# Optimization experiments

Measured on AMD Instinct MI355X. Metric: run time of the kernel, lower is better.

Reference implementation:

```python
import jax, jax.numpy as jnp
import numpy as np

S, B, D, H, E, K = 1024, 4, 1024, 16, 3, 2
DFF = 4 * D
DH = D // H


def _layernorm(x, w, b, eps=1e-5):
    mu = jnp.mean(x, axis=-1, keepdims=True)
    var = jnp.var(x, axis=-1, keepdims=True)
    return (x - mu) * jax.lax.rsqrt(var + eps) * w + b


def _quick_gelu(x):
    return x * jax.nn.sigmoid(1.702 * x)


def setup_inputs() -> dict:
    key = jax.random.key(0)
    ks = jax.random.split(key, 8)
    w = lambda k, shape: jax.random.normal(k, shape, dtype=jnp.float32) * 0.02
    return {
        "x": jax.random.normal(ks[0], (S, B, D), dtype=jnp.float32),
        "ln1_w": jnp.ones((D,), jnp.float32), "ln1_b": jnp.zeros((D,), jnp.float32),
        "ln2_w": jnp.ones((D,), jnp.float32), "ln2_b": jnp.zeros((D,), jnp.float32),
        "in_proj_w": w(ks[1], (3 * D, D)), "in_proj_b": jnp.zeros((3 * D,), jnp.float32),
        "out_proj_w": w(ks[2], (D, D)), "out_proj_b": jnp.zeros((D,), jnp.float32),
        "gate_w": w(ks[3], (E, D)),
        "fc_w": w(ks[4], (E, DFF, D)), "fc_b": jnp.zeros((E, DFF), jnp.float32),
        "proj_w": w(ks[5], (E, D, DFF)), "proj_b": jnp.zeros((E, D), jnp.float32),
    }


def _forward(x, ln1_w, ln1_b, ln2_w, ln2_b, in_proj_w, in_proj_b,
             out_proj_w, out_proj_b, gate_w, fc_w, fc_b, proj_w, proj_b):
    s, b, d = x.shape
    # --- causal self-attention (torch nn.MultiheadAttention, seq-first) ---
    h = _layernorm(x, ln1_w, ln1_b)
    qkv = h @ in_proj_w.T + in_proj_b                      # [S,B,3D]
    q, k, v = jnp.split(qkv, 3, axis=-1)
    to_bhsd = lambda t: t.reshape(s, b, H, DH).transpose(1, 2, 0, 3)  # [B,H,S,Dh]
    q, k, v = to_bhsd(q) * (DH ** -0.5), to_bhsd(k), to_bhsd(v)
    mask = jnp.where(jnp.arange(s)[:, None] >= jnp.arange(s)[None, :], 0.0, -jnp.inf)
    scores = jnp.einsum("bhqd,bhkd->bhqk", q, k) + mask    # [B,H,S,S]
    attn = jax.nn.softmax(scores, axis=-1)
    o = jnp.einsum("bhqk,bhkd->bhqd", attn, v)
    o = o.transpose(2, 0, 1, 3).reshape(s, b, d)
    x = x + (o @ out_proj_w.T + out_proj_b)

    # --- MoE routing ---
    hs = _layernorm(x, ln2_w, ln2_b)
    hs_flat = hs.reshape(-1, d)                            # [T,D], T = S*B
    router_logits = hs_flat @ gate_w.T                     # [T,E]
    rw = jax.nn.softmax(router_logits.astype(jnp.float32), axis=-1)
    top_vals, top_idx = jax.lax.top_k(rw, K)               # [T,K]
    top_vals = top_vals / jnp.sum(top_vals, axis=-1, keepdims=True)

    # dense grouped expert FFN (E=3 small, compute-all + masked combine)
    h1 = _quick_gelu(jnp.einsum("td,efd->etf", hs_flat, fc_w) + fc_b[:, None, :])
    expert_out = jnp.einsum("etf,edf->etd", h1, proj_w) + proj_b[:, None, :]  # [E,T,D]
    comb = jnp.sum(jax.nn.one_hot(top_idx, E, dtype=top_vals.dtype) * top_vals[..., None], axis=1)  # [T,E]
    final_hidden_states = jnp.einsum("te,etd->td", comb, expert_out).reshape(s, b, d)
    del final_hidden_states  # NOTE: source computes this but never uses it in the output

    gate_score = jnp.max(top_vals, axis=-1).reshape(s, b, 1)
    out = x * gate_score
    return out, router_logits


def reference(x, ln1_w, ln1_b, ln2_w, ln2_b, in_proj_w, in_proj_b,
              out_proj_w, out_proj_b, gate_w, fc_w, fc_b, proj_w, proj_b):
    return _forward(x, ln1_w, ln1_b, ln2_w, ln2_b, in_proj_w, in_proj_b,
                    out_proj_w, out_proj_b, gate_w, fc_w, fc_b, proj_w, proj_b)
```

## Files before the change

kernel.cpp:

```cpp
#include <hip/hip_runtime.h>
#include <hip/hip_bf16.h>

#define S_DIM 1024
#define B_DIM 4
#define D_DIM 1024
#define H_DIM 16
#define DH    64
#define T_DIM (S_DIM * B_DIM)
#define QKV_N (3 * D_DIM)

using bf16 = __hip_bfloat16;
typedef __attribute__((ext_vector_type(4))) float fx4;
typedef __attribute__((ext_vector_type(8))) short bx8;

__device__ __forceinline__ unsigned short f2bf(float f) {
  union { float f; unsigned int u; } cv; cv.f = f;
  unsigned int u = cv.u;
  unsigned int r = (u + 0x7FFFu + ((u >> 16) & 1u)) >> 16;
  return (unsigned short)r;
}

__device__ __forceinline__ void g2l16(const void* g, void* l) {
  __builtin_amdgcn_global_load_lds(
      (const __attribute__((address_space(1))) unsigned int*)g,
      (__attribute__((address_space(3))) unsigned int*)l, 16, 0, 0);
}

__global__ __launch_bounds__(256) void cast2_f32_bf16(
    const float* __restrict__ a, bf16* __restrict__ da, int an4,
    const float* __restrict__ b, bf16* __restrict__ db, int bn4) {
  const int i = blockIdx.x * 256 + threadIdx.x;
  const float* src; bf16* dst; int j;
  if (i < an4) { src = a; dst = da; j = i; }
  else if (i < an4 + bn4) { src = b; dst = db; j = i - an4; }
  else return;
  const fx4 v = ((const fx4*)src)[j];
  ushort4 u;
  u.x = f2bf(v[0]); u.y = f2bf(v[1]); u.z = f2bf(v[2]); u.w = f2bf(v[3]);
  ((ushort4*)dst)[j] = u;
}

__global__ __launch_bounds__(256) void ln_bf16_kernel(
    const float* __restrict__ x, const float* __restrict__ w,
    const float* __restrict__ bb, bf16* __restrict__ out) {
  const int t = blockIdx.x, tid = threadIdx.x;
  const fx4 v = ((const fx4*)(x + (size_t)t * D_DIM))[tid];
  float s  = v[0] + v[1] + v[2] + v[3];
  float ss = v[0]*v[0] + v[1]*v[1] + v[2]*v[2] + v[3]*v[3];
#pragma unroll
  for (int off = 32; off >= 1; off >>= 1) {
    s  += __shfl_xor(s, off);
    ss += __shfl_xor(ss, off);
  }
  __shared__ float red[8];
  const int wid = tid >> 6, lane = tid & 63;
  if (lane == 0) { red[wid] = s; red[4 + wid] = ss; }
  __syncthreads();
  s  = red[0] + red[1] + red[2] + red[3];
  ss = red[4] + red[5] + red[6] + red[7];
  const float mu = s * (1.f / D_DIM);
  const float rstd = rsqrtf(ss * (1.f / D_DIM) - mu * mu + 1e-5f);
  const fx4 wv = ((const fx4*)w)[tid];
  const fx4 bv = ((const fx4*)bb)[tid];
  ushort4 u;
  u.x = f2bf((v[0] - mu) * rstd * wv[0] + bv[0]);
  u.y = f2bf((v[1] - mu) * rstd * wv[1] + bv[1]);
  u.z = f2bf((v[2] - mu) * rstd * wv[2] + bv[2]);
  u.w = f2bf((v[3] - mu) * rstd * wv[3] + bv[3]);
  ((ushort4*)(out + (size_t)t * D_DIM))[tid] = u;
}

template <int EPI>
__global__ __launch_bounds__(256, 2) void gemm_bt(
    const bf16* __restrict__ A, const bf16* __restrict__ B,
    const float* __restrict__ bias, const float* __restrict__ resid,
    float* __restrict__ C, ushort* __restrict__ qkvb, int N, int K) {
  __shared__ bf16 sA[2][128 * 32];
  __shared__ bf16 sB[2][128 * 32];
  const int tid  = threadIdx.x;
  const int brow = blockIdx.y * 128;
  const int bcol = blockIdx.x * 128;
  const int wid  = tid >> 6;
  const int lane = tid & 63;
  const int wr   = wid >> 1;
  const int wc   = wid & 1;
  const int fr   = lane & 15;
  const int fk   = lane >> 4;

  fx4 acc[4][4];
#pragma unroll
  for (int i = 0; i < 4; ++i)
#pragma unroll
    for (int j = 0; j < 4; ++j) acc[i][j] = 0.f;

  const int arow = tid >> 2;
  const int acol = (tid & 3) * 8;

  auto stage = [&](int buf, int kt) {
#pragma unroll
    for (int is = 0; is < 2; ++is) {
      const int row = is * 64 + arow;
      const int off = row * 64 + acol * 2;
      g2l16(A + (size_t)(brow + row) * K + kt + acol, (char*)sA[buf] + off);
      g2l16(B + (size_t)(bcol + row) * K + kt + acol, (char*)sB[buf] + off);
    }
  };

  stage(0, 0);
  asm volatile("s_waitcnt vmcnt(0)" ::: "memory");
  __builtin_amdgcn_s_barrier();
  asm volatile("" ::: "memory");

  const int nk = K >> 5;
  int cur = 0;
#pragma unroll 1
  for (int ki = 0; ki < nk; ++ki) {
    if (ki + 1 < nk) stage(cur ^ 1, (ki + 1) * 32);
    asm volatile("" ::: "memory");

    bx8 af[4], bfr[4];
#pragma unroll
    for (int mm = 0; mm < 4; ++mm)
      af[mm] = *(const bx8*)(sA[cur] + (wr * 64 + mm * 16 + fr) * 32 + fk * 8);
#pragma unroll
    for (int nn = 0; nn < 4; ++nn)
      bfr[nn] = *(const bx8*)(sB[cur] + (wc * 64 + nn * 16 + fr) * 32 + fk * 8);
#pragma unroll
    for (int mm = 0; mm < 4; ++mm)
#pragma unroll
      for (int nn = 0; nn < 4; ++nn)
        acc[mm][nn] = __builtin_amdgcn_mfma_f32_16x16x32_bf16(
            af[mm], bfr[nn], acc[mm][nn], 0, 0, 0);

    if (ki + 1 < nk) {
      asm volatile("s_waitcnt vmcnt(0)" ::: "memory");
      __builtin_amdgcn_s_barrier();
      asm volatile("" ::: "memory");
    }
    cur ^= 1;
  }

  const int row0 = brow + wr * 64 + fk * 4;
  const int col0 = bcol + wc * 64 + fr;
#pragma unroll
  for (int mm = 0; mm < 4; ++mm) {
#pragma unroll
    for (int nn = 0; nn < 4; ++nn) {
      const int col = col0 + nn * 16;
      const float bv = bias[col];
      if (EPI == 1) {
#pragma unroll
        for (int rr = 0; rr < 4; ++rr) {
          const int row = row0 + mm * 16 + rr;
          C[(size_t)row * N + col] = acc[mm][nn][rr] + bv + resid[(size_t)row * N + col];
        }
      } else {
        const int which = col >> 10;
        const int rem   = col & 1023;
        const int hh    = rem >> 6;
        const int dh    = rem & 63;
        const float scale = (which == 0) ? 0.18033688f : 1.0f;
#pragma unroll
        for (int rr = 0; rr < 4; ++rr) {
          const int row = row0 + mm * 16 + rr;
          const int ss2 = row >> 2, bb2 = row & 3;
          const float v = (acc[mm][nn][rr] + bv) * scale;
          qkvb[(size_t)which * 4194304 +
               ((size_t)(bb2 * 16 + hh)) * 65536 + (size_t)ss2 * 64 + dh] = f2bf(v);
        }
      }
    }
  }
}

__global__ __launch_bounds__(256) void transpose_v(
    const ushort* __restrict__ v, ushort* __restrict__ vt) {
  __shared__ ushort tile[64][65];
  const int g  = blockIdx.x;
  const int bh = g >> 4, st = g & 15;
  const int s0 = st * 64;
  const int tid = threadIdx.x;
  const int r  = tid >> 2;
  const int c0 = (tid & 3) * 16;
  const ushort* src = v + (size_t)bh * 65536 + (size_t)(s0 + r) * 64 + c0;
#pragma unroll
  for (int i = 0; i < 2; ++i) {
    const bx8 d = *(const bx8*)(src + i * 8);
#pragma unroll
    for (int j = 0; j < 8; ++j) tile[r][c0 + i * 8 + j] = (ushort)d[j];
  }
  __syncthreads();
  ushort* dst = vt + (size_t)bh * 65536 + (size_t)r * 1024 + s0 + c0;
  bx8 w0, w1;
#pragma unroll
  for (int j = 0; j < 8; ++j) {
    w0[j] = (short)tile[c0 + j][r];
    w1[j] = (short)tile[c0 + 8 + j][r];
  }
  *(bx8*)dst = w0;
  *(bx8*)(dst + 8) = w1;
}

__global__ __launch_bounds__(256, 4) void attn_mfma(
    const ushort* __restrict__ qb, const ushort* __restrict__ kb,
    const ushort* __restrict__ vtb, ushort* __restrict__ ob) {
  __shared__ __align__(16) char sK[2][8192];
  __shared__ __align__(16) char sVT[2][8192];
  __shared__ __align__(16) char sP[8192];
  const int tid  = threadIdx.x;
  const int wid  = tid >> 6;
  const int lane = tid & 63;
  const int g    = blockIdx.x;
  const int qt   = 15 - (g >> 6);
  const int bh   = g & 63;
  const int b    = bh >> 4, h = bh & 15;
  const int fr   = lane & 15;
  const int fk   = lane >> 4;
  const size_t bhoff = (size_t)bh * 65536;
  char* const sPw = sP + wid * 2048;
  const int swp = (fr & 7) << 4;

  auto stage = [&](int buf, int k0) {
#pragma unroll
    for (int is = 0; is < 2; ++is) {
      const int L    = is * 4096 + tid * 16;
      const int row  = L >> 7;
      const int colb = (L & 127) ^ ((row & 7) << 4);
      g2l16(kb  + bhoff + (size_t)(k0 + row) * 64 + (colb >> 1), sK[buf]  + L);
      g2l16(vtb + bhoff + (size_t)row * 1024 + k0 + (colb >> 1), sVT[buf] + L);
    }
  };

  const int q0w = qt * 64 + wid * 16;
  const ushort* qp = qb + bhoff + (size_t)(q0w + fr) * 64;
  const bx8 qf0 = *(const bx8*)(qp + fk * 8);
  const bx8 qf1 = *(const bx8*)(qp + 32 + fk * 8);
  asm volatile("s_waitcnt vmcnt(0)" ::: "memory");

  fx4 o4[4];
  float m = -3e38f, l = 0.f;
#pragma unroll
  for (int dt = 0; dt < 4; ++dt) o4[dt] = 0.f;

  stage(0, 0);
  int cur = 0;

#pragma unroll 1
  for (int kbk = 0; kbk <= qt; ++kbk) {
    if (kbk < qt) {
      stage(cur ^ 1, (kbk + 1) * 64);
      asm volatile("s_waitcnt vmcnt(4)" ::: "memory");
    } else {
      asm volatile("s_waitcnt vmcnt(0)" ::: "memory");
    }
    __builtin_amdgcn_s_barrier();
    asm volatile("" ::: "memory");
    const char* sKc  = sK[cur];
    const char* sVTc = sVT[cur];

    fx4 s4[4];
    __builtin_amdgcn_s_setprio(1);
#pragma unroll
    for (int kt = 0; kt < 4; ++kt) {
      const int krow = kt * 16 + fr;
      const int sw   = (krow & 7) << 4;
      const bx8 kf0 = *(const bx8*)(sKc + krow * 128 + ((fk * 16) ^ sw));
      const bx8 kf1 = *(const bx8*)(sKc + krow * 128 + ((64 + fk * 16) ^ sw));
      fx4 z = {0.f, 0.f, 0.f, 0.f};
      z = __builtin_amdgcn_mfma_f32_16x16x32_bf16(kf0, qf0, z, 0, 0, 0);
      s4[kt] = __builtin_amdgcn_mfma_f32_16x16x32_bf16(kf1, qf1, z, 0, 0, 0);
    }
    __builtin_amdgcn_s_setprio(0);

    if (kbk == qt) {
      const int qloc = wid * 16 + fr;
#pragma unroll
      for (int kt = 0; kt < 4; ++kt) {
        const int keyb = kt * 16 + fk * 4;
#pragma unroll
        for (int rr = 0; rr < 4; ++rr)
          if (keyb + rr > qloc) s4[kt][rr] = -3e38f;
      }
    }

    float pm = s4[0][0];
#pragma unroll
    for (int kt = 0; kt < 4; ++kt)
#pragma unroll
      for (int rr = 0; rr < 4; ++rr) pm = fmaxf(pm, s4[kt][rr]);
    pm = fmaxf(pm, __shfl_xor(pm, 16));
    pm = fmaxf(pm, __shfl_xor(pm, 32));

    if (__any(pm > m + 11.5f)) {
      const float mn = fmaxf(m, pm);
      const float f  = exp2f(m - mn);
      m = mn;
      l *= f;
      float fq[4];
#pragma unroll
      for (int rr = 0; rr < 4; ++rr) fq[rr] = __shfl(f, fk * 4 + rr);
#pragma unroll
      for (int dt = 0; dt < 4; ++dt)
#pragma unroll
        for (int rr = 0; rr < 4; ++rr) o4[dt][rr] *= fq[rr];
    }

#pragma unroll
    for (int kt = 0; kt < 4; ++kt) {
      union { float f; unsigned u; } a0, a1, a2, a3;
      a0.f = exp2f(s4[kt][0] - m);
      a1.f = exp2f(s4[kt][1] - m);
      a2.f = exp2f(s4[kt][2] - m);
      a3.f = exp2f(s4[kt][3] - m);
      l += (a0.f + a1.f) + (a2.f + a3.f);
      uint2 pk;
      pk.x = (a0.u >> 16) | (a1.u & 0xFFFF0000u);
      pk.y = (a2.u >> 16) | (a3.u & 0xFFFF0000u);
      *(uint2*)(sPw + ((fr * 128 + kt * 32 + fk * 8) ^ swp)) = pk;
    }

    __builtin_amdgcn_s_setprio(1);
#pragma unroll
    for (int c = 0; c < 2; ++c) {
      const bx8 pa = *(const bx8*)(sPw + ((fr * 128 + c * 64 + fk * 16) ^ swp));
#pragma unroll
      for (int dt = 0; dt < 4; ++dt) {
        const int vrow = dt * 16 + fr;
        const bx8 vf = *(const bx8*)(sVTc + vrow * 128 +
                                     ((c * 64 + fk * 16) ^ ((vrow & 7) << 4)));
        o4[dt] = __builtin_amdgcn_mfma_f32_16x16x32_bf16(pa, vf, o4[dt], 0, 0, 0);
      }
    }
    __builtin_amdgcn_s_setprio(0);

    asm volatile("" ::: "memory");
    __builtin_amdgcn_s_barrier();
    asm volatile("" ::: "memory");
    cur ^= 1;
  }

  l += __shfl_xor(l, 16);
  l += __shfl_xor(l, 32);
  const float linv = 1.f / l;
  float lq[4];
#pragma unroll
  for (int rr = 0; rr < 4; ++rr) lq[rr] = __shfl(linv, fk * 4 + rr);

#pragma unroll
  for (int dt = 0; dt < 4; ++dt) {
#pragma unroll
    for (int rr = 0; rr < 4; ++rr) {
      const int qq = q0w + fk * 4 + rr;
      ob[((size_t)qq * 4 + b) * 1024 + h * 64 + dt * 16 + fr] =
          f2bf(o4[dt][rr] * lq[rr]);
    }
  }
}

__global__ __launch_bounds__(256) void final_kernel(
    const float* __restrict__ xn, const float* __restrict__ w,
    const float* __restrict__ bb, const float* __restrict__ gw,
    float* __restrict__ out, float* __restrict__ rlog) {
  const int t = blockIdx.x, tid = threadIdx.x;
  const fx4 v = ((const fx4*)(xn + (size_t)t * D_DIM))[tid];
  float s  = v[0] + v[1] + v[2] + v[3];
  float ss = v[0]*v[0] + v[1]*v[1] + v[2]*v[2] + v[3]*v[3];
#pragma unroll
  for (int off = 32; off >= 1; off >>= 1) {
    s  += __shfl_xor(s, off);
    ss += __shfl_xor(ss, off);
  }
  __shared__ float red[8];
  __shared__ float red2[12];
  const int wid = tid >> 6, lane = tid & 63;
  if (lane == 0) { red[wid] = s; red[4 + wid] = ss; }
  __syncthreads();
  s  = red[0] + red[1] + red[2] + red[3];
  ss = red[4] + red[5] + red[6] + red[7];
  const float mu = s * (1.f / D_DIM);
  const float rstd = rsqrtf(ss * (1.f / D_DIM) - mu * mu + 1e-5f);
  const fx4 wv = ((const fx4*)w)[tid];
  const fx4 bv = ((const fx4*)bb)[tid];
  fx4 hv;
#pragma unroll
  for (int cc = 0; cc < 4; ++cc) hv[cc] = (v[cc] - mu) * rstd * wv[cc] + bv[cc];

  const fx4 w0 = ((const fx4*)(gw           ))[tid];
  const fx4 w1 = ((const fx4*)(gw +     D_DIM))[tid];
  const fx4 w2 = ((const fx4*)(gw + 2 * D_DIM))[tid];
  float g0 = hv[0]*w0[0] + hv[1]*w0[1] + hv[2]*w0[2] + hv[3]*w0[3];
  float g1 = hv[0]*w1[0] + hv[1]*w1[1] + hv[2]*w1[2] + hv[3]*w1[3];
  float g2 = hv[0]*w2[0] + hv[1]*w2[1] + hv[2]*w2[2] + hv[3]*w2[3];
#pragma unroll
  for (int off = 32; off >= 1; off >>= 1) {
    g0 += __shfl_xor(g0, off);
    g1 += __shfl_xor(g1, off);
    g2 += __shfl_xor(g2, off);
  }
  if (lane == 0) { red2[wid] = g0; red2[4 + wid] = g1; red2[8 + wid] = g2; }
  __syncthreads();
  g0 = red2[0] + red2[1] + red2[2]  + red2[3];
  g1 = red2[4] + red2[5] + red2[6]  + red2[7];
  g2 = red2[8] + red2[9] + red2[10] + red2[11];

  const float lmax = fmaxf(g0, fmaxf(g1, g2));
  const float lmin = fminf(g0, fminf(g1, g2));
  const float lmid = (g0 + g1 + g2) - lmax - lmin;
  const float gate = 1.f / (1.f + __expf(lmid - lmax));

  ((fx4*)(out + (size_t)t * D_DIM))[tid] = v * gate;
  if (tid == 0) {
    rlog[(size_t)t * 3 + 0] = g0;
    rlog[(size_t)t * 3 + 1] = g1;
    rlog[(size_t)t * 3 + 2] = g2;
  }
}

extern "C" void kernel_launch(void* const* d_in, const int* in_sizes, int n_in,
                              void* d_out, int out_size, void* d_ws, size_t ws_size,
                              hipStream_t stream) {
  (void)in_sizes; (void)n_in; (void)out_size; (void)ws_size;
  const float* x    = (const float*)d_in[0];
  const float* ln1w = (const float*)d_in[1];
  const float* ln1b = (const float*)d_in[2];
  const float* ln2w = (const float*)d_in[3];
  const float* ln2b = (const float*)d_in[4];
  const float* win  = (const float*)d_in[5];
  const float* bin  = (const float*)d_in[6];
  const float* wout = (const float*)d_in[7];
  const float* bout = (const float*)d_in[8];
  const float* gw   = (const float*)d_in[9];

  char* ws = (char*)d_ws;
  bf16*   w_in_b  = (bf16*)(ws);
  bf16*   w_out_b = (bf16*)(ws + 6291456);
  bf16*   h_b     = (bf16*)(ws + 8388608);
  ushort* o_b     = (ushort*)h_b;
  ushort* qkvb    = (ushort*)(ws + 16777216);
  ushort* q_b     = qkvb;
  ushort* k_b     = qkvb + 4194304;
  ushort* v_b     = qkvb + 8388608;
  float*  xnew    = (float*)(ws + 41943040);
  ushort* vt_b    = (ushort*)(ws + 58720256);

  float* out  = (float*)d_out;
  float* rlog = out + (size_t)T_DIM * D_DIM;

  cast2_f32_bf16<<<4096, 256, 0, stream>>>(win, w_in_b, 786432,
                                           wout, w_out_b, 262144);
  ln_bf16_kernel<<<T_DIM, 256, 0, stream>>>(x, ln1w, ln1b, h_b);
  gemm_bt<2><<<dim3(QKV_N / 128, T_DIM / 128), 256, 0, stream>>>(
      h_b, w_in_b, bin, nullptr, nullptr, qkvb, QKV_N, D_DIM);
  transpose_v<<<1024, 256, 0, stream>>>(v_b, vt_b);
  attn_mfma<<<1024, 256, 0, stream>>>(q_b, k_b, vt_b, o_b);
  gemm_bt<1><<<dim3(D_DIM / 128, T_DIM / 128), 256, 0, stream>>>(
      (const bf16*)o_b, w_out_b, bout, x, xnew, nullptr, D_DIM, D_DIM);
  final_kernel<<<T_DIM, 256, 0, stream>>>(xnew, ln2w, ln2b, gw, out, rlog);
}
```

Measured before the change: 115.8 us.

## Use 256x128 tiles for QKV GEMM and k-major LDS layout

```diff
diff --git a/kernel.cpp b/kernel.cpp
--- a/kernel.cpp
+++ b/kernel.cpp
@@ -70,13 +70,111 @@
   ((ushort4*)(out + (size_t)t * D_DIM))[tid] = u;
 }
 
-template <int EPI>
+__global__ __launch_bounds__(256, 2) void gemm_qkv(
+    const bf16* __restrict__ A, const bf16* __restrict__ B,
+    const float* __restrict__ bias, ushort* __restrict__ qkvb, int N, int K) {
+  __shared__ char sA[2][16384];
+  __shared__ char sB[2][8192];
+  const int tid  = threadIdx.x;
+  const int brow = blockIdx.y * 256;
+  const int bcol = blockIdx.x * 128;
+  const int wid  = tid >> 6;
+  const int lane = tid & 63;
+  const int wr   = wid >> 1;
+  const int wc   = wid & 1;
+  const int fr   = lane & 15;
+  const int fk   = lane >> 4;
+
+  fx4 acc[8][4];
+#pragma unroll
+  for (int i = 0; i < 8; ++i)
+#pragma unroll
+    for (int j = 0; j < 4; ++j) acc[i][j] = 0.f;
+
+  auto stage = [&](int buf, int kt) {
+#pragma unroll
+    for (int is = 0; is < 4; ++is) {
+      const int o = is * 4096 + tid * 16;
+      const int fkg = o >> 12;
+      const int row = (o & 4095) >> 4;
+      g2l16(A + (size_t)(brow + row) * K + kt + fkg * 8, sA[buf] + o);
+    }
+#pragma unroll
+    for (int is = 0; is < 2; ++is) {
+      const int o = is * 4096 + tid * 16;
+      const int fkg = o >> 11;
+      const int row = (o & 2047) >> 4;
+      g2l16(B + (size_t)(bcol + row) * K + kt + fkg * 8, sB[buf] + o);
+    }
+  };
+
+  stage(0, 0);
+  asm volatile("s_waitcnt vmcnt(0)" ::: "memory");
+  __builtin_amdgcn_s_barrier();
+  asm volatile("" ::: "memory");
+
+  const int nk = K >> 5;
+  int cur = 0;
+#pragma unroll 1
+  for (int ki = 0; ki < nk; ++ki) {
+    if (ki + 1 < nk) stage(cur ^ 1, (ki + 1) * 32);
+    asm volatile("" ::: "memory");
+
+    bx8 af[8], bfr[4];
+#pragma unroll
+    for (int mm = 0; mm < 8; ++mm)
+      af[mm] = *(const bx8*)(sA[cur] + fk * 4096 + (wr * 128 + mm * 16 + fr) * 16);
+#pragma unroll
+    for (int nn = 0; nn < 4; ++nn)
+      bfr[nn] = *(const bx8*)(sB[cur] + fk * 2048 + (wc * 64 + nn * 16 + fr) * 16);
+    __builtin_amdgcn_s_setprio(1);
+#pragma unroll
+    for (int mm = 0; mm < 8; ++mm)
+#pragma unroll
+      for (int nn = 0; nn < 4; ++nn)
+        acc[mm][nn] = __builtin_amdgcn_mfma_f32_16x16x32_bf16(
+            af[mm], bfr[nn], acc[mm][nn], 0, 0, 0);
+    __builtin_amdgcn_s_setprio(0);
+
+    if (ki + 1 < nk) {
+      asm volatile("s_waitcnt vmcnt(0)" ::: "memory");
+      __builtin_amdgcn_s_barrier();
+      asm volatile("" ::: "memory");
+    }
+    cur ^= 1;
+  }
+
+  const int row0 = brow + wr * 128 + fk * 4;
+  const int col0 = bcol + wc * 64 + fr;
+#pragma unroll
+  for (int mm = 0; mm < 8; ++mm) {
+#pragma unroll
+    for (int nn = 0; nn < 4; ++nn) {
+      const int col = col0 + nn * 16;
+      const float bv = bias[col];
+      const int which = col >> 10;
+      const int rem   = col & 1023;
+      const int hh    = rem >> 6;
+      const int dh    = rem & 63;
+      const float scale = (which == 0) ? 0.18033688f : 1.0f;
+#pragma unroll
+      for (int rr = 0; rr < 4; ++rr) {
+        const int row = row0 + mm * 16 + rr;
+        const int ss2 = row >> 2, bb2 = row & 3;
+        const float v = (acc[mm][nn][rr] + bv) * scale;
+        qkvb[(size_t)which * 4194304 +
+             ((size_t)(bb2 * 16 + hh)) * 65536 + (size_t)ss2 * 64 + dh] = f2bf(v);
+      }
+    }
+  }
+}
+
 __global__ __launch_bounds__(256, 2) void gemm_bt(
     const bf16* __restrict__ A, const bf16* __restrict__ B,
     const float* __restrict__ bias, const float* __restrict__ resid,
-    float* __restrict__ C, ushort* __restrict__ qkvb, int N, int K) {
-  __shared__ bf16 sA[2][128 * 32];
-  __shared__ bf16 sB[2][128 * 32];
+    float* __restrict__ C, int N, int K) {
+  __shared__ char sA[2][8192];
+  __shared__ char sB[2][8192];
   const int tid  = threadIdx.x;
   const int brow = blockIdx.y * 128;
   const int bcol = blockIdx.x * 128;
@@ -93,16 +191,14 @@
 #pragma unroll
     for (int j = 0; j < 4; ++j) acc[i][j] = 0.f;
 
-  const int arow = tid >> 2;
-  const int acol = (tid & 3) * 8;
-
   auto stage = [&](int buf, int kt) {
 #pragma unroll
     for (int is = 0; is < 2; ++is) {
-      const int row = is * 64 + arow;
-      const int off = row * 64 + acol * 2;
-      g2l16(A + (size_t)(brow + row) * K + kt + acol, (char*)sA[buf] + off);
-      g2l16(B + (size_t)(bcol + row) * K + kt + acol, (char*)sB[buf] + off);
+      const int o = is * 4096 + tid * 16;
+      const int fkg = o >> 11;
+      const int row = (o & 2047) >> 4;
+      g2l16(A + (size_t)(brow + row) * K + kt + fkg * 8, sA[buf] + o);
+      g2l16(B + (size_t)(bcol + row) * K + kt + fkg * 8, sB[buf] + o);
     }
   };
 
@@ -121,10 +217,10 @@
     bx8 af[4], bfr[4];
 #pragma unroll
     for (int mm = 0; mm < 4; ++mm)
-      af[mm] = *(const bx8*)(sA[cur] + (wr * 64 + mm * 16 + fr) * 32 + fk * 8);
+      af[mm] = *(const bx8*)(sA[cur] + fk * 2048 + (wr * 64 + mm * 16 + fr) * 16);
 #pragma unroll
     for (int nn = 0; nn < 4; ++nn)
-      bfr[nn] = *(const bx8*)(sB[cur] + (wc * 64 + nn * 16 + fr) * 32 + fk * 8);
+      bfr[nn] = *(const bx8*)(sB[cur] + fk * 2048 + (wc * 64 + nn * 16 + fr) * 16);
 #pragma unroll
     for (int mm = 0; mm < 4; ++mm)
 #pragma unroll
@@ -148,26 +244,10 @@
     for (int nn = 0; nn < 4; ++nn) {
       const int col = col0 + nn * 16;
       const float bv = bias[col];
-      if (EPI == 1) {
-#pragma unroll
-        for (int rr = 0; rr < 4; ++rr) {
-          const int row = row0 + mm * 16 + rr;
-          C[(size_t)row * N + col] = acc[mm][nn][rr] + bv + resid[(size_t)row * N + col];
-        }
-      } else {
-        const int which = col >> 10;
-        const int rem   = col & 1023;
-        const int hh    = rem >> 6;
-        const int dh    = rem & 63;
-        const float scale = (which == 0) ? 0.18033688f : 1.0f;
-#pragma unroll
-        for (int rr = 0; rr < 4; ++rr) {
-          const int row = row0 + mm * 16 + rr;
-          const int ss2 = row >> 2, bb2 = row & 3;
-          const float v = (acc[mm][nn][rr] + bv) * scale;
-          qkvb[(size_t)which * 4194304 +
-               ((size_t)(bb2 * 16 + hh)) * 65536 + (size_t)ss2 * 64 + dh] = f2bf(v);
-        }
+#pragma unroll
+      for (int rr = 0; rr < 4; ++rr) {
+        const int row = row0 + mm * 16 + rr;
+        C[(size_t)row * N + col] = acc[mm][nn][rr] + bv + resid[(size_t)row * N + col];
       }
     }
   }
@@ -449,11 +529,11 @@
   cast2_f32_bf16<<<4096, 256, 0, stream>>>(win, w_in_b, 786432,
                                            wout, w_out_b, 262144);
   ln_bf16_kernel<<<T_DIM, 256, 0, stream>>>(x, ln1w, ln1b, h_b);
-  gemm_bt<2><<<dim3(QKV_N / 128, T_DIM / 128), 256, 0, stream>>>(
-      h_b, w_in_b, bin, nullptr, nullptr, qkvb, QKV_N, D_DIM);
+  gemm_qkv<<<dim3(QKV_N / 128, T_DIM / 256), 256, 0, stream>>>(
+      h_b, w_in_b, bin, qkvb, QKV_N, D_DIM);
   transpose_v<<<1024, 256, 0, stream>>>(v_b, vt_b);
   attn_mfma<<<1024, 256, 0, stream>>>(q_b, k_b, vt_b, o_b);
-  gemm_bt<1><<<dim3(D_DIM / 128, T_DIM / 128), 256, 0, stream>>>(
-      (const bf16*)o_b, w_out_b, bout, x, xnew, nullptr, D_DIM, D_DIM);
+  gemm_bt<<<dim3(D_DIM / 128, T_DIM / 128), 256, 0, stream>>>(
+      (const bf16*)o_b, w_out_b, bout, x, xnew, D_DIM, D_DIM);
   final_kernel<<<T_DIM, 256, 0, stream>>>(xnew, ln2w, ln2b, gw, out, rlog);
 }
```

Result: slower. 148.0 us (+27.8%).
